# Kernel tuning notes

Hardware: AMD Instinct MI355X
Metric: run time of the kernel (lower is better)

## Reference

```python
import jax, jax.numpy as jnp
import numpy as np
from jax import lax

SEQ, B, NF, NC, D, NO, L = 2036, 32, 64, 100, 512, 4, 2048
EPS = 1e-5


def leaky(x):
    return jnp.where(x > 0, x, 0.2 * x)


def conv1d(x, w, b):
    # x: [B, Cin, L], w: [Cout, Cin, K] -> [B, Cout, L-K+1] (VALID)
    y = lax.conv_general_dilated(x, w, (1,), 'VALID',
                                 dimension_numbers=('NCH', 'OIH', 'NCH'))
    return y + b[None, :, None]


def maxpool3(x):
    # kernel 3, stride 1, VALID, over last dim
    return lax.reduce_window(x, -jnp.inf, lax.max, (1, 1, 3), (1, 1, 1), 'VALID')


def layernorm(x, g, b):
    m = jnp.mean(x, -1, keepdims=True)
    v = jnp.mean(jnp.square(x - m), -1, keepdims=True)
    return (x - m) * lax.rsqrt(v + EPS) * g + b


def setup_inputs() -> dict:
    key = jax.random.key(0)
    ks = jax.random.split(key, 16)
    s = 0.02
    return {
        'input': jax.random.normal(ks[0], (SEQ, B, NF), jnp.float32),
        'history': jax.random.normal(ks[1], (B, NO, L), jnp.float32),
        'static': jax.random.normal(ks[2], (B, NC), jnp.float32),
        'W_feat': jax.random.normal(ks[3], (D, NF), jnp.float32) * s,
        'b_feat': jnp.zeros((D,), jnp.float32),
        'w1': jax.random.normal(ks[4], (D // 4, NO, 3), jnp.float32) * s,
        'b1': jnp.zeros((D // 4,), jnp.float32),
        'w2': jax.random.normal(ks[5], (D // 2, D // 4, 3), jnp.float32) * s,
        'b2': jnp.zeros((D // 2,), jnp.float32),
        'w3': jax.random.normal(ks[6], (D, D // 2, 3), jnp.float32) * s,
        'b3': jnp.zeros((D,), jnp.float32),
        'g1': jnp.ones((D,), jnp.float32),
        'beta1': jnp.zeros((D,), jnp.float32),
        'W_city': jax.random.normal(ks[7], (D, NC), jnp.float32) * s,
        'b_city': jnp.zeros((D,), jnp.float32),
        'g2': jnp.ones((D,), jnp.float32),
        'beta2': jnp.zeros((D,), jnp.float32),
    }


def reference(input, history, static, W_feat, b_feat, w1, b1, w2, b2, w3, b3,
              g1, beta1, W_city, b_city, g2, beta2):
    # feat embed: [S, B, NF] @ [NF, D]
    x = leaky(jnp.einsum('sbf,df->sbd', input, W_feat) + b_feat)
    # conv/pool stack on history [B, NO, L]
    h = maxpool3(leaky(conv1d(history, w1, b1)))
    h = maxpool3(leaky(conv1d(h, w2, b2)))
    h = maxpool3(leaky(conv1d(h, w3, b3)))            # [B, D, S]
    x = x + jnp.transpose(h, (2, 0, 1))               # [S, B, D]
    x = layernorm(x, g1, beta1)
    # diag_embed(city_embed(static)) matmul == broadcasted elementwise scale
    c = static @ W_city.T + b_city                    # [B, D]
    x = x * c[None, :, :]
    x = layernorm(x, g2, beta2)
    return x
```

## Files before the change

kernel.cpp:

```cpp
#include <hip/hip_runtime.h>
#include <hip/hip_bf16.h>

#define SEQ 2036
#define BB 32
#define DDIM 512
#define PREP_BLOCKS 2112

typedef __attribute__((ext_vector_type(4))) float f32x4;
typedef __attribute__((ext_vector_type(8))) short bf16x8v;
typedef __attribute__((ext_vector_type(8))) unsigned short u16x8;
typedef __attribute__((ext_vector_type(4))) unsigned short u16x4;

__device__ __forceinline__ float leaky_f(float x) { return x > 0.f ? x : 0.2f * x; }
__device__ __forceinline__ unsigned short f2bf(float x) {
    unsigned u = __float_as_uint(x);
    return (unsigned short)((u + 0x7fffu + ((u >> 16) & 1u)) >> 16);
}
__device__ __forceinline__ float bf2f(unsigned short h) { return __uint_as_float(((unsigned)h) << 16); }

#define GLOAD_LDS16(g, l)                                                                  \
    __builtin_amdgcn_global_load_lds((__attribute__((address_space(1))) const unsigned int*)(g), \
                                     (__attribute__((address_space(3))) unsigned int*)(l), 16, 0, 0)

__global__ __launch_bounds__(256) void pre_kernel(
    const float* __restrict__ w2, __hip_bfloat16* __restrict__ w2P,
    const float* __restrict__ w3, __hip_bfloat16* __restrict__ wb3,
    const float* __restrict__ Wf, __hip_bfloat16* __restrict__ wfP,
    const float* __restrict__ st, const float* __restrict__ Wc,
    const float* __restrict__ bc, float* __restrict__ cv,
    const float* __restrict__ hist, const float* __restrict__ w1,
    const float* __restrict__ b1, __hip_bfloat16* __restrict__ h1)
{
    __shared__ float t1[4][68];
    const int t = threadIdx.x;
    if (blockIdx.x < PREP_BLOCKS) {
        int idx = blockIdx.x * 256 + t;
        if (idx < 98304) {
            int o = idx & 4095, tile = idx >> 12;
            int nb = tile % 2;
            int tmp = tile / 2;
            int q = tmp % 4, k = tmp / 4;
            int n = o >> 5, low = o & 31;
            int cs = low >> 3, j = low & 7;
            int c = cs ^ ((n >> 1) & 3);
            int kk = (c << 3) | j;
            float v = w2[((size_t)(nb * 128 + n)) * 128 * 3 + (q * 32 + kk) * 3 + k];
            ((unsigned short*)w2P)[idx] = f2bf(v);
            return;
        }
        idx -= 98304;
        if (idx < 393216) {
            int e = idx & 7;
            int l = (idx >> 3) & 63;
            int nf = (idx >> 9) & 3;
            int wn = (idx >> 11) & 1;
            int rest = idx >> 12;
            int nb = rest % 4, ss = rest / 4;
            int k = (ss % 12) >> 2;
            int qg = (ss / 12) * 4 + (ss & 3);
            int n = nb * 128 + wn * 64 + nf * 16 + (l & 15);
            int cin = qg * 32 + (l >> 4) * 8 + e;
            ((unsigned short*)wb3)[idx] = f2bf(w3[(size_t)n * 256 * 3 + cin * 3 + k]);
            return;
        }
        idx -= 393216;
        if (idx < 32768) {
            int e = idx & 7;
            int l = (idx >> 3) & 63;
            int frag = idx >> 9;
            int q = frag >> 5, j = frag & 31;
            int n = l & 15, g = l >> 4;
            ((unsigned short*)wfP)[idx] = f2bf(Wf[(j * 16 + n) * 64 + q * 32 + g * 8 + e]);
            return;
        }
        idx -= 32768;
        if (idx < 16384) {
            int b = idx >> 9, d = idx & 511;
            const float* sb = st + b * 100;
            float acc = bc[d];
#pragma unroll 4
            for (int f = 0; f < 100; ++f) acc = fmaf(sb[f], Wc[d * 100 + f], acc);
            cv[b * 512 + d] = acc;
        }
        return;
    }
    const int cb = blockIdx.x - PREP_BLOCKS;
    const int b = cb >> 5, tile = cb & 31;
    const int d = t & 127, sub = t >> 7;
    const int sbase = tile * 64;
    const float* inb = hist + (size_t)b * 4 * 2048;
    for (int i = t; i < 4 * 68; i += 256) {
        int cin = i / 68, p = i - cin * 68;
        int s = sbase + p;
        t1[cin][p] = (s < 2048) ? inb[cin * 2048 + s] : 0.f;
    }
    __syncthreads();
    float acc[34];
#pragma unroll
    for (int i = 0; i < 34; ++i) acc[i] = 0.f;
#pragma unroll
    for (int cin = 0; cin < 4; ++cin) {
        float w0 = w1[d * 12 + cin * 3 + 0];
        float w1v = w1[d * 12 + cin * 3 + 1];
        float w2v = w1[d * 12 + cin * 3 + 2];
        float r0 = t1[cin][sub * 32], r1 = t1[cin][sub * 32 + 1];
#pragma unroll
        for (int p = 0; p < 34; ++p) {
            float r2 = t1[cin][sub * 32 + p + 2];
            acc[p] = fmaf(r0, w0, fmaf(r1, w1v, fmaf(r2, w2v, acc[p])));
            r0 = r1; r1 = r2;
        }
    }
    const float bvv = b1[d];
    unsigned short* o16 = (unsigned short*)h1;
#pragma unroll
    for (int i = 0; i < 32; ++i) {
        int sp = sbase + sub * 32 + i;
        if (sp < 2044) {
            float v = leaky_f(fmaxf(fmaxf(acc[i], acc[i + 1]), acc[i + 2]) + bvv);
            o16[((size_t)b * 2044 + sp) * 128 + d] = f2bf(v);
        }
    }
}

template <int CIN, int DOUT, bool LDSB>
__global__ __launch_bounds__(256, LDSB ? 3 : 4) void conv_mfma_kernel(
    const __hip_bfloat16* __restrict__ hin,
    const __hip_bfloat16* __restrict__ wprep,
    const float* __restrict__ bias,
    __hip_bfloat16* __restrict__ hout,
    int Lin, int Lpool, long bstride, long sstride)
{
    constexpr int NQ = CIN / 32;
    constexpr int HALVES = (CIN + 127) / 128;
    constexpr int NSTEP = 3 * NQ;
    constexpr int SPH = NSTEP / HALVES;
    constexpr int NBL = DOUT / 128;
    constexpr int SMEM = LDSB ? (34816 + 16384) : 34816;

    __shared__ __attribute__((aligned(16))) unsigned char smem[SMEM];
    unsigned char* panel = smem;
    unsigned char* cstage = smem;
    unsigned char* bls = smem + 34816;

    const int t = threadIdx.x;
    const int lane = t & 63, w = t >> 6;
    const int wr = w >> 1, wn = w & 1;
    const int l15 = lane & 15, lg = lane >> 4;

    const int nwg = gridDim.x;
    const int lw = (blockIdx.x & 7) * (nwg >> 3) + (blockIdx.x >> 3);
    const int nb = lw % NBL;
    const int tmp = lw / NBL;
    const int st = tmp % 17;
    const int b = tmp / 17;
    const int s0 = st * 126;

    auto stage_panel = [&](int half) {
        const char* srcb = (const char*)hin + (((size_t)b * Lin) * CIN + half * 128) * 2;
#pragma unroll
        for (int iter = 0; iter < 8; ++iter) {
            int chunk = iter * 256 + t;
            int r = chunk >> 4, cd = chunk & 15;
            int c = (cd & 8) | ((cd ^ r) & 7);
            int row = s0 + r; if (row > Lin - 1) row = Lin - 1;
            const char* src = srcb + ((size_t)row * CIN + c * 8) * 2;
            GLOAD_LDS16(src, panel + (iter * 256 + w * 64) * 16);
        }
        if (t < 32) {
            int chunk = 2048 + t;
            int r = chunk >> 4, cd = chunk & 15;
            int c = (cd & 8) | ((cd ^ r) & 7);
            int row = s0 + r; if (row > Lin - 1) row = Lin - 1;
            const char* src = srcb + ((size_t)row * CIN + c * 8) * 2;
            GLOAD_LDS16(src, panel + 2048 * 16);
        }
    };

    f32x4 acc[4][4];
#pragma unroll
    for (int i = 0; i < 4; ++i)
#pragma unroll
        for (int j = 0; j < 4; ++j) acc[i][j] = (f32x4){0.f, 0.f, 0.f, 0.f};

    const int rbse = wr * 64 + l15;

    if (LDSB) {
        auto stage_b = [&](int ss, int bi) {
            int k = (ss % SPH) >> 2;
            int qg = (ss / SPH) * 4 + (ss & 3);
            int tile = (k * NQ + qg) * NBL + nb;
            const char* src = (const char*)wprep + (size_t)tile * 8192;
            char* dst = (char*)bls + bi * 8192;
            GLOAD_LDS16(src + t * 16, dst + (w << 10));
            GLOAD_LDS16(src + 4096 + t * 16, dst + 4096 + (w << 10));
        };
        stage_panel(0);
        stage_b(0, 0);
        __syncthreads();
        int boff[4];
#pragma unroll
        for (int nf = 0; nf < 4; ++nf) {
            int n = wn * 64 + nf * 16 + l15;
            boff[nf] = n * 64 + ((lg ^ ((n >> 1) & 3)) << 4);
        }
        for (int ss = 0; ss < NSTEP; ++ss) {
            const int bi = ss & 1;
            if (ss + 1 < NSTEP) stage_b(ss + 1, bi ^ 1);
            const int k = (ss % SPH) >> 2;
            const int cc = (ss & 3) * 4 + lg;
            bf16x8v a[4], bfr[4];
#pragma unroll
            for (int mf = 0; mf < 4; ++mf) {
                int r = rbse + mf * 16 + k;
                int csw = (cc & 8) | ((cc ^ r) & 7);
                a[mf] = *(const bf16x8v*)(panel + r * 256 + (csw << 4));
            }
#pragma unroll
            for (int nf = 0; nf < 4; ++nf)
                bfr[nf] = *(const bf16x8v*)(bls + bi * 8192 + boff[nf]);
#pragma unroll
            for (int mf = 0; mf < 4; ++mf)
#pragma unroll
                for (int nf = 0; nf < 4; ++nf)
                    acc[mf][nf] = __builtin_amdgcn_mfma_f32_16x16x32_bf16(a[mf], bfr[nf], acc[mf][nf], 0, 0, 0);
            __syncthreads();
            if (HALVES == 2 && ss == SPH - 1) {
                stage_panel(1);
                __syncthreads();
            }
        }
        __syncthreads();
    } else {
        const unsigned short* wbp = (const unsigned short*)wprep;
        auto kstep = [&](int ss) {
            const int k = (ss % SPH) >> 2;
            const int cc = (ss & 3) * 4 + lg;
            const unsigned short* wq =
                wbp + (((size_t)ss * NBL + nb) * 2 + wn) * 2048 + (size_t)lane * 8;
            bf16x8v a[4], bfr[4];
#pragma unroll
            for (int nf = 0; nf < 4; ++nf)
                bfr[nf] = *(const bf16x8v*)(wq + nf * 512);
#pragma unroll
            for (int mf = 0; mf < 4; ++mf) {
                int r = rbse + mf * 16 + k;
                int csw = (cc & 8) | ((cc ^ r) & 7);
                a[mf] = *(const bf16x8v*)(panel + r * 256 + (csw << 4));
            }
#pragma unroll
            for (int mf = 0; mf < 4; ++mf)
#pragma unroll
                for (int nf = 0; nf < 4; ++nf)
                    acc[mf][nf] = __builtin_amdgcn_mfma_f32_16x16x32_bf16(a[mf], bfr[nf], acc[mf][nf], 0, 0, 0);
        };
        stage_panel(0);
        __syncthreads();
        for (int ss = 0; ss < SPH; ++ss) kstep(ss);
        if (HALVES == 2) {
            __syncthreads();
            stage_panel(1);
            __syncthreads();
            for (int ss = SPH; ss < NSTEP; ++ss) kstep(ss);
        }
        __syncthreads();
    }

#pragma unroll
    for (int mf = 0; mf < 4; ++mf) {
        int srow = wr * 64 + mf * 16 + (lg << 2);
#pragma unroll
        for (int nf = 0; nf < 4; ++nf) {
            int n = wn * 64 + nf * 16 + l15;
            f32x4 v = acc[mf][nf];
            unsigned lo = (unsigned)f2bf(v.x) | ((unsigned)f2bf(v.y) << 16);
            unsigned hi = (unsigned)f2bf(v.z) | ((unsigned)f2bf(v.w) << 16);
            *(uint2*)(cstage + (size_t)n * 272 + srow * 2) = make_uint2(lo, hi);
        }
    }
    __syncthreads();

    const int n = t & 127, h = t >> 7;
    const float bv = bias[nb * 128 + n];
    const int SP = (Lpool - s0 < 126) ? (Lpool - s0) : 126;
    const int splo = h ? 63 : 0;
    const int sphim = h ? 126 : 63;
    const int sphi = (SP < sphim) ? SP : sphim;
    const int cbg = h ? 7 : 0, ceg = h ? 16 : 9;
    unsigned short* outp = (unsigned short*)hout;
    const size_t obase = (size_t)b * bstride + (size_t)s0 * sstride + nb * 128 + n;
    float p2 = 0.f, p1 = 0.f;
    for (int j = cbg; j < ceg; ++j) {
        u16x8 ch = *(const u16x8*)(cstage + (size_t)n * 272 + (j << 4));
#pragma unroll
        for (int i = 0; i < 8; ++i) {
            float cur = bf2f(ch[i]);
            int sp = j * 8 + i - 2;
            if (sp >= splo && sp < sphi) {
                float v = fmaxf(fmaxf(p2, p1), cur) + bv;
                outp[obase + (size_t)sp * sstride] = f2bf(leaky_f(v));
            }
            p2 = p1; p1 = cur;
        }
    }
}

#define XSTR 514
__global__ __launch_bounds__(256, 4) void epi_mfma3_kernel(
    const float* __restrict__ input,
    const __hip_bfloat16* __restrict__ wfP,
    const float* __restrict__ bfeat,
    const __hip_bfloat16* __restrict__ h3,
    const float* __restrict__ cvec,
    const float* __restrict__ g1, const float* __restrict__ be1,
    const float* __restrict__ g2, const float* __restrict__ be2,
    float* __restrict__ outp)
{
    __shared__ float x_lds[16 * XSTR];
    const int t = threadIdx.x;
    const int lane = t & 63, w = t >> 6;
    const int l15 = lane & 15, lg = lane >> 4;
    const long r0 = (long)blockIdx.x * 16;

    f32x4 acc[8];
#pragma unroll
    for (int jl = 0; jl < 8; ++jl) acc[jl] = (f32x4){0.f, 0.f, 0.f, 0.f};

    const unsigned short* wp = (const unsigned short*)wfP;
#pragma unroll
    for (int q = 0; q < 2; ++q) {
        const f32x4* ap = (const f32x4*)(input + (r0 + l15) * 64 + q * 32 + lg * 8);
        f32x4 a0 = ap[0];
        f32x4 a1 = ap[1];
        bf16x8v af;
        af[0] = (short)f2bf(a0.x); af[1] = (short)f2bf(a0.y);
        af[2] = (short)f2bf(a0.z); af[3] = (short)f2bf(a0.w);
        af[4] = (short)f2bf(a1.x); af[5] = (short)f2bf(a1.y);
        af[6] = (short)f2bf(a1.z); af[7] = (short)f2bf(a1.w);
#pragma unroll
        for (int jl = 0; jl < 8; ++jl) {
            int frag = q * 32 + w * 8 + jl;
            bf16x8v bfr = *(const bf16x8v*)(wp + ((size_t)frag * 64 + lane) * 8);
            acc[jl] = __builtin_amdgcn_mfma_f32_16x16x32_bf16(af, bfr, acc[jl], 0, 0, 0);
        }
    }

#pragma unroll
    for (int jl = 0; jl < 8; ++jl) {
        int d = (w * 8 + jl) * 16 + l15;
        float bfv = bfeat[d];
#pragma unroll
        for (int i = 0; i < 4; ++i) {
            int row = lg * 4 + i;
            x_lds[row * XSTR + d] = leaky_f(acc[jl][i] + bfv);
        }
    }
    __syncthreads();

    const unsigned short* h3u = (const unsigned short*)h3;
    const int l4 = lane * 4;
    f32x4 g1a = *(const f32x4*)(g1 + l4);
    f32x4 g1b = *(const f32x4*)(g1 + 256 + l4);
    f32x4 b1a = *(const f32x4*)(be1 + l4);
    f32x4 b1b = *(const f32x4*)(be1 + 256 + l4);
    f32x4 g2a = *(const f32x4*)(g2 + l4);
    f32x4 g2b = *(const f32x4*)(g2 + 256 + l4);
    f32x4 b2a = *(const f32x4*)(be2 + l4);
    f32x4 b2b = *(const f32x4*)(be2 + 256 + l4);

    for (int rr = 0; rr < 4; ++rr) {
        int row = w * 4 + rr;
        long r = r0 + row;
        int b = (int)(r & 31);
        f32x4 xa = *(const f32x4*)(x_lds + row * XSTR + l4);
        f32x4 xb = *(const f32x4*)(x_lds + row * XSTR + 256 + l4);
        u16x4 ha = *(const u16x4*)(h3u + r * 512 + l4);
        u16x4 hb = *(const u16x4*)(h3u + r * 512 + 256 + l4);
        float v[8];
        float s = 0.f;
#pragma unroll
        for (int e = 0; e < 4; ++e) {
            v[e] = xa[e] + bf2f(ha[e]);
            v[4 + e] = xb[e] + bf2f(hb[e]);
            s += v[e] + v[4 + e];
        }
#pragma unroll
        for (int off = 32; off; off >>= 1) s += __shfl_xor(s, off);
        float m = s * (1.f / 512.f);
        float vs = 0.f;
#pragma unroll
        for (int j = 0; j < 8; ++j) { float dd = v[j] - m; vs += dd * dd; }
#pragma unroll
        for (int off = 32; off; off >>= 1) vs += __shfl_xor(vs, off);
        float rstd = rsqrtf(vs * (1.f / 512.f) + 1e-5f);

        f32x4 ca = *(const f32x4*)(cvec + b * 512 + l4);
        f32x4 cb = *(const f32x4*)(cvec + b * 512 + 256 + l4);
        float z[8]; float s2 = 0.f;
#pragma unroll
        for (int e = 0; e < 4; ++e) {
            z[e] = ((v[e] - m) * rstd * g1a[e] + b1a[e]) * ca[e];
            z[4 + e] = ((v[4 + e] - m) * rstd * g1b[e] + b1b[e]) * cb[e];
            s2 += z[e] + z[4 + e];
        }
#pragma unroll
        for (int off = 32; off; off >>= 1) s2 += __shfl_xor(s2, off);
        float m2 = s2 * (1.f / 512.f);
        float vs2 = 0.f;
#pragma unroll
        for (int j = 0; j < 8; ++j) { float dd = z[j] - m2; vs2 += dd * dd; }
#pragma unroll
        for (int off = 32; off; off >>= 1) vs2 += __shfl_xor(vs2, off);
        float rstd2 = rsqrtf(vs2 * (1.f / 512.f) + 1e-5f);

        f32x4 oa, ob;
#pragma unroll
        for (int e = 0; e < 4; ++e) {
            oa[e] = (z[e] - m2) * rstd2 * g2a[e] + b2a[e];
            ob[e] = (z[4 + e] - m2) * rstd2 * g2b[e] + b2b[e];
        }
        __builtin_nontemporal_store(oa, (f32x4*)(outp + r * 512 + l4));
        __builtin_nontemporal_store(ob, (f32x4*)(outp + r * 512 + 256 + l4));
    }
}

extern "C" void kernel_launch(void* const* d_in, const int* in_sizes, int n_in,
                              void* d_out, int out_size, void* d_ws, size_t ws_size,
                              hipStream_t stream) {
    const float* input   = (const float*)d_in[0];
    const float* history = (const float*)d_in[1];
    const float* stat    = (const float*)d_in[2];
    const float* W_feat  = (const float*)d_in[3];
    const float* b_feat  = (const float*)d_in[4];
    const float* w1      = (const float*)d_in[5];
    const float* b1      = (const float*)d_in[6];
    const float* w2      = (const float*)d_in[7];
    const float* b2      = (const float*)d_in[8];
    const float* w3      = (const float*)d_in[9];
    const float* b3      = (const float*)d_in[10];
    const float* g1      = (const float*)d_in[11];
    const float* beta1   = (const float*)d_in[12];
    const float* W_city  = (const float*)d_in[13];
    const float* b_city  = (const float*)d_in[14];
    const float* g2      = (const float*)d_in[15];
    const float* beta2   = (const float*)d_in[16];
    float* out = (float*)d_out;

    char* wsb = (char*)d_ws;
    size_t off = 0;
    auto alloc = [&](size_t bytes) {
        void* p = wsb + off;
        off = (off + bytes + 255) & ~(size_t)255;
        return p;
    };
    __hip_bfloat16* h1  = (__hip_bfloat16*)alloc((size_t)BB * 2044 * 128 * 2);
    __hip_bfloat16* h2  = (__hip_bfloat16*)alloc((size_t)BB * 2040 * 256 * 2);
    __hip_bfloat16* h3  = (__hip_bfloat16*)alloc((size_t)SEQ * BB * 512 * 2);
    float*          cv  = (float*)alloc((size_t)BB * DDIM * 4);
    __hip_bfloat16* w2P = (__hip_bfloat16*)alloc((size_t)98304 * 2);
    __hip_bfloat16* wb3 = (__hip_bfloat16*)alloc((size_t)393216 * 2);
    __hip_bfloat16* wfP = (__hip_bfloat16*)alloc((size_t)32768 * 2);

    pre_kernel<<<PREP_BLOCKS + 1024, 256, 0, stream>>>(
        w2, w2P, w3, wb3, W_feat, wfP, stat, W_city, b_city, cv,
        history, w1, b1, h1);

    conv_mfma_kernel<128, 256, true><<<17 * 2 * BB, 256, 0, stream>>>(
        h1, w2P, b2, h2, 2044, 2040, 2040L * 256, 256);
    conv_mfma_kernel<256, 512, false><<<17 * 4 * BB, 256, 0, stream>>>(
        h2, wb3, b3, h3, 2040, 2036, 512, 32L * 512);

    epi_mfma3_kernel<<<(SEQ * BB) / 16, 256, 0, stream>>>(
        input, wfP, b_feat, h3, cv, g1, beta1, g2, beta2, out);
}
```

Measured before the change: 171.0 us.

## Shrink conv tiles to 64 rows with 128-thread blocks reading weights from global

Both conv layers now use one kernel with 128-thread blocks that each cover 62 pooled positions instead of 126. The panel and staging buffers shrink to 18 KB. Conv2 drops its LDS double-buffered weight staging and, like conv3, loads pre-swizzled bf16 fragments straight from global memory. The goal is more blocks, higher occupancy and less LDS and barrier overhead, at the cost of more halo recomputation and more repeated weight reads per output.

```diff
diff --git a/kernel.cpp b/kernel.cpp
--- a/kernel.cpp
+++ b/kernel.cpp
@@ -23,7 +23,7 @@
                                      (__attribute__((address_space(3))) unsigned int*)(l), 16, 0, 0)
 
 __global__ __launch_bounds__(256) void pre_kernel(
-    const float* __restrict__ w2, __hip_bfloat16* __restrict__ w2P,
+    const float* __restrict__ w2, __hip_bfloat16* __restrict__ wb2,
     const float* __restrict__ w3, __hip_bfloat16* __restrict__ wb3,
     const float* __restrict__ Wf, __hip_bfloat16* __restrict__ wfP,
     const float* __restrict__ st, const float* __restrict__ Wc,
@@ -36,16 +36,17 @@
     if (blockIdx.x < PREP_BLOCKS) {
         int idx = blockIdx.x * 256 + t;
         if (idx < 98304) {
-            int o = idx & 4095, tile = idx >> 12;
-            int nb = tile % 2;
-            int tmp = tile / 2;
-            int q = tmp % 4, k = tmp / 4;
-            int n = o >> 5, low = o & 31;
-            int cs = low >> 3, j = low & 7;
-            int c = cs ^ ((n >> 1) & 3);
-            int kk = (c << 3) | j;
-            float v = w2[((size_t)(nb * 128 + n)) * 128 * 3 + (q * 32 + kk) * 3 + k];
-            ((unsigned short*)w2P)[idx] = f2bf(v);
+            int e = idx & 7;
+            int l = (idx >> 3) & 63;
+            int nf = (idx >> 9) & 3;
+            int w = (idx >> 11) & 1;
+            int rest = idx >> 12;
+            int nb = rest % 2, ss = rest / 2;
+            int k = ss >> 2;
+            int qg = ss & 3;
+            int n = nb * 128 + w * 64 + nf * 16 + (l & 15);
+            int cin = qg * 32 + (l >> 4) * 8 + e;
+            ((unsigned short*)wb2)[idx] = f2bf(w2[(size_t)n * 384 + cin * 3 + k]);
             return;
         }
         idx -= 98304;
@@ -53,14 +54,14 @@
             int e = idx & 7;
             int l = (idx >> 3) & 63;
             int nf = (idx >> 9) & 3;
-            int wn = (idx >> 11) & 1;
+            int w = (idx >> 11) & 1;
             int rest = idx >> 12;
             int nb = rest % 4, ss = rest / 4;
             int k = (ss % 12) >> 2;
             int qg = (ss / 12) * 4 + (ss & 3);
-            int n = nb * 128 + wn * 64 + nf * 16 + (l & 15);
+            int n = nb * 128 + w * 64 + nf * 16 + (l & 15);
             int cin = qg * 32 + (l >> 4) * 8 + e;
-            ((unsigned short*)wb3)[idx] = f2bf(w3[(size_t)n * 256 * 3 + cin * 3 + k]);
+            ((unsigned short*)wb3)[idx] = f2bf(w3[(size_t)n * 768 + cin * 3 + k]);
             return;
         }
         idx -= 393216;
@@ -123,57 +124,51 @@
     }
 }
 
-template <int CIN, int DOUT, bool LDSB>
-__global__ __launch_bounds__(256, LDSB ? 3 : 4) void conv_mfma_kernel(
+template <int CIN, int NBL>
+__global__ __launch_bounds__(128, 4) void conv_sm_kernel(
     const __hip_bfloat16* __restrict__ hin,
-    const __hip_bfloat16* __restrict__ wprep,
+    const __hip_bfloat16* __restrict__ wb,
     const float* __restrict__ bias,
     __hip_bfloat16* __restrict__ hout,
     int Lin, int Lpool, long bstride, long sstride)
 {
-    constexpr int NQ = CIN / 32;
-    constexpr int HALVES = (CIN + 127) / 128;
-    constexpr int NSTEP = 3 * NQ;
-    constexpr int SPH = NSTEP / HALVES;
-    constexpr int NBL = DOUT / 128;
-    constexpr int SMEM = LDSB ? (34816 + 16384) : 34816;
-
-    __shared__ __attribute__((aligned(16))) unsigned char smem[SMEM];
+    constexpr int HALVES = CIN / 128;
+    constexpr int NSTEP = 3 * (CIN / 32);
+
+    __shared__ __attribute__((aligned(16))) unsigned char smem[18432];
     unsigned char* panel = smem;
     unsigned char* cstage = smem;
-    unsigned char* bls = smem + 34816;
 
     const int t = threadIdx.x;
     const int lane = t & 63, w = t >> 6;
-    const int wr = w >> 1, wn = w & 1;
     const int l15 = lane & 15, lg = lane >> 4;
 
     const int nwg = gridDim.x;
     const int lw = (blockIdx.x & 7) * (nwg >> 3) + (blockIdx.x >> 3);
     const int nb = lw % NBL;
     const int tmp = lw / NBL;
-    const int st = tmp % 17;
-    const int b = tmp / 17;
-    const int s0 = st * 126;
+    const int st = tmp % 33;
+    const int b = tmp / 33;
+    const int s0 = st * 62;
 
     auto stage_panel = [&](int half) {
         const char* srcb = (const char*)hin + (((size_t)b * Lin) * CIN + half * 128) * 2;
 #pragma unroll
         for (int iter = 0; iter < 8; ++iter) {
-            int chunk = iter * 256 + t;
+            int chunk = iter * 128 + t;
             int r = chunk >> 4, cd = chunk & 15;
             int c = (cd & 8) | ((cd ^ r) & 7);
             int row = s0 + r; if (row > Lin - 1) row = Lin - 1;
             const char* src = srcb + ((size_t)row * CIN + c * 8) * 2;
-            GLOAD_LDS16(src, panel + (iter * 256 + w * 64) * 16);
+            GLOAD_LDS16(src, panel + (iter * 128 + w * 64) * 16);
         }
         if (t < 32) {
-            int chunk = 2048 + t;
+            int chunk = 1024 + t;
             int r = chunk >> 4, cd = chunk & 15;
             int c = (cd & 8) | ((cd ^ r) & 7);
             int row = s0 + r; if (row > Lin - 1) row = Lin - 1;
             const char* src = srcb + ((size_t)row * CIN + c * 8) * 2;
-            GLOAD_LDS16(src, panel + 2048 * 16);
+            GLOAD_LDS16(src, panel + 1024 * 16);
         }
     };
 
@@ -183,120 +178,68 @@
 #pragma unroll
         for (int j = 0; j < 4; ++j) acc[i][j] = (f32x4){0.f, 0.f, 0.f, 0.f};
 
-    const int rbse = wr * 64 + l15;
-
-    if (LDSB) {
-        auto stage_b = [&](int ss, int bi) {
-            int k = (ss % SPH) >> 2;
-            int qg = (ss / SPH) * 4 + (ss & 3);
-            int tile = (k * NQ + qg) * NBL + nb;
-            const char* src = (const char*)wprep + (size_t)tile * 8192;
-            char* dst = (char*)bls + bi * 8192;
-            GLOAD_LDS16(src + t * 16, dst + (w << 10));
-            GLOAD_LDS16(src + 4096 + t * 16, dst + 4096 + (w << 10));
-        };
-        stage_panel(0);
-        stage_b(0, 0);
+    const unsigned short* wbp = (const unsigned short*)wb;
+    auto kstep = [&](int ss) {
+        const int k = (ss % 12) >> 2;
+        const int cc = (ss & 3) * 4 + lg;
+        const unsigned short* wq =
+            wbp + (((size_t)ss * NBL + nb) * 2 + w) * 2048 + (size_t)lane * 8;
+        bf16x8v a[4], bfr[4];
+#pragma unroll
+        for (int nf = 0; nf < 4; ++nf)
+            bfr[nf] = *(const bf16x8v*)(wq + nf * 512);
+#pragma unroll
+        for (int mf = 0; mf < 4; ++mf) {
+            int r = l15 + mf * 16 + k;
+            int csw = (cc & 8) | ((cc ^ r) & 7);
+            a[mf] = *(const bf16x8v*)(panel + r * 256 + (csw << 4));
+        }
+#pragma unroll
+        for (int mf = 0; mf < 4; ++mf)
+#pragma unroll
+            for (int nf = 0; nf < 4; ++nf)
+                acc[mf][nf] = __builtin_amdgcn_mfma_f32_16x16x32_bf16(a[mf], bfr[nf], acc[mf][nf], 0, 0, 0);
+    };
+
+    stage_panel(0);
+    __syncthreads();
+    for (int ss = 0; ss < 12; ++ss) kstep(ss);
+    if (HALVES == 2) {
         __syncthreads();
-        int boff[4];
+        stage_panel(1);
+        __syncthreads();
+        for (int ss = 12; ss < NSTEP; ++ss) kstep(ss);
+    }
+    __syncthreads();
+
+#pragma unroll
+    for (int mf = 0; mf < 4; ++mf) {
+        int srow = mf * 16 + (lg << 2);
 #pragma unroll
         for (int nf = 0; nf < 4; ++nf) {
-            int n = wn * 64 + nf * 16 + l15;
-            boff[nf] = n * 64 + ((lg ^ ((n >> 1) & 3)) << 4);
-        }
-        for (int ss = 0; ss < NSTEP; ++ss) {
-            const int bi = ss & 1;
-            if (ss + 1 < NSTEP) stage_b(ss + 1, bi ^ 1);
-            const int k = (ss % SPH) >> 2;
-            const int cc = (ss & 3) * 4 + lg;
-            bf16x8v a[4], bfr[4];
-#pragma unroll
-            for (int mf = 0; mf < 4; ++mf) {
-                int r = rbse + mf * 16 + k;
-                int csw = (cc & 8) | ((cc ^ r) & 7);
-                a[mf] = *(const bf16x8v*)(panel + r * 256 + (csw << 4));
-            }
-#pragma unroll
-            for (int nf = 0; nf < 4; ++nf)
-                bfr[nf] = *(const bf16x8v*)(bls + bi * 8192 + boff[nf]);
-#pragma unroll
-            for (int mf = 0; mf < 4; ++mf)
-#pragma unroll
-                for (int nf = 0; nf < 4; ++nf)
-                    acc[mf][nf] = __builtin_amdgcn_mfma_f32_16x16x32_bf16(a[mf], bfr[nf], acc[mf][nf], 0, 0, 0);
-            __syncthreads();
-            if (HALVES == 2 && ss == SPH - 1) {
-                stage_panel(1);
-                __syncthreads();
-            }
-        }
-        __syncthreads();
-    } else {
-        const unsigned short* wbp = (const unsigned short*)wprep;
-        auto kstep = [&](int ss) {
-            const int k = (ss % SPH) >> 2;
-            const int cc = (ss & 3) * 4 + lg;
-            const unsigned short* wq =
-                wbp + (((size_t)ss * NBL + nb) * 2 + wn) * 2048 + (size_t)lane * 8;
-            bf16x8v a[4], bfr[4];
-#pragma unroll
-            for (int nf = 0; nf < 4; ++nf)
-                bfr[nf] = *(const bf16x8v*)(wq + nf * 512);
-#pragma unroll
-            for (int mf = 0; mf < 4; ++mf) {
-                int r = rbse + mf * 16 + k;
-                int csw = (cc & 8) | ((cc ^ r) & 7);
-                a[mf] = *(const bf16x8v*)(panel + r * 256 + (csw << 4));
-            }
-#pragma unroll
-            for (int mf = 0; mf < 4; ++mf)
-#pragma unroll
-                for (int nf = 0; nf < 4; ++nf)
-                    acc[mf][nf] = __builtin_amdgcn_mfma_f32_16x16x32_bf16(a[mf], bfr[nf], acc[mf][nf], 0, 0, 0);
-        };
-        stage_panel(0);
-        __syncthreads();
-        for (int ss = 0; ss < SPH; ++ss) kstep(ss);
-        if (HALVES == 2) {
-            __syncthreads();
-            stage_panel(1);
-            __syncthreads();
-            for (int ss = SPH; ss < NSTEP; ++ss) kstep(ss);
-        }
-        __syncthreads();
-    }
-
-#pragma unroll
-    for (int mf = 0; mf < 4; ++mf) {
-        int srow = wr * 64 + mf * 16 + (lg << 2);
-#pragma unroll
-        for (int nf = 0; nf < 4; ++nf) {
-            int n = wn * 64 + nf * 16 + l15;
+            int n = w * 64 + nf * 16 + l15;
             f32x4 v = acc[mf][nf];
             unsigned lo = (unsigned)f2bf(v.x) | ((unsigned)f2bf(v.y) << 16);
             unsigned hi = (unsigned)f2bf(v.z) | ((unsigned)f2bf(v.w) << 16);
-            *(uint2*)(cstage + (size_t)n * 272 + srow * 2) = make_uint2(lo, hi);
+            *(uint2*)(cstage + (size_t)n * 144 + srow * 2) = make_uint2(lo, hi);
         }
     }
     __syncthreads();
 
-    const int n = t & 127, h = t >> 7;
+    const int n = t;
     const float bv = bias[nb * 128 + n];
-    const int SP = (Lpool - s0 < 126) ? (Lpool - s0) : 126;
-    const int splo = h ? 63 : 0;
-    const int sphim = h ? 126 : 63;
-    const int sphi = (SP < sphim) ? SP : sphim;
-    const int cbg = h ? 7 : 0, ceg = h ? 16 : 9;
+    const int SP = (Lpool - s0 < 62) ? (Lpool - s0) : 62;
     unsigned short* outp = (unsigned short*)hout;
     const size_t obase = (size_t)b * bstride + (size_t)s0 * sstride + nb * 128 + n;
     float p2 = 0.f, p1 = 0.f;
-    for (int j = cbg; j < ceg; ++j) {
-        u16x8 ch = *(const u16x8*)(cstage + (size_t)n * 272 + (j << 4));
+#pragma unroll
+    for (int j = 0; j < 8; ++j) {
+        u16x8 ch = *(const u16x8*)(cstage + (size_t)n * 144 + (j << 4));
 #pragma unroll
         for (int i = 0; i < 8; ++i) {
             float cur = bf2f(ch[i]);
             int sp = j * 8 + i - 2;
-            if (sp >= splo && sp < sphi) {
+            if ((unsigned)sp < (unsigned)SP) {
                 float v = fmaxf(fmaxf(p2, p1), cur) + bv;
                 outp[obase + (size_t)sp * sstride] = f2bf(leaky_f(v));
             }
@@ -457,18 +400,19 @@
     __hip_bfloat16* h2  = (__hip_bfloat16*)alloc((size_t)BB * 2040 * 256 * 2);
     __hip_bfloat16* h3  = (__hip_bfloat16*)alloc((size_t)SEQ * BB * 512 * 2);
     float*          cv  = (float*)alloc((size_t)BB * DDIM * 4);
-    __hip_bfloat16* w2P = (__hip_bfloat16*)alloc((size_t)98304 * 2);
+    __hip_bfloat16* wb2 = (__hip_bfloat16*)alloc((size_t)98304 * 2);
     __hip_bfloat16* wb3 = (__hip_bfloat16*)alloc((size_t)393216 * 2);
     __hip_bfloat16* wfP = (__hip_bfloat16*)alloc((size_t)32768 * 2);
 
     pre_kernel<<<PREP_BLOCKS + 1024, 256, 0, stream>>>(
-        w2, w2P, w3, wb3, W_feat, wfP, stat, W_city, b_city, cv,
+        w2, wb2, w3, wb3, W_feat, wfP, stat, W_city, b_city, cv,
         history, w1, b1, h1);
 
-    conv_mfma_kernel<128, 256, true><<<17 * 2 * BB, 256, 0, stream>>>(
-        h1, w2P, b2, h2, 2044, 2040, 2040L * 256, 256);
-    conv_mfma_kernel<256, 512, false><<<17 * 4 * BB, 256, 0, stream>>>(
-        h2, wb3, b3, h3, 2040, 2036, 512, 32L * 512);
+    conv_sm_kernel<128, 2><<<33 * 2 * BB, 128, 0, stream>>>(
+        h1, wb2, b2, h2, 2044, 2040, 2040L * 256, 256);
+
+    conv_sm_kernel<256, 4><<<33 * 4 * BB, 128, 0, stream>>>(
+        h2, wb3, b3, h3, 2040, 2036, 512, 16384);
 
     epi_mfma3_kernel<<<(SEQ * BB) / 16, 256, 0, stream>>>(
         input, wfP, b_feat, h3, cv, g1, beta1, g2, beta2, out);
```

Measured after the change: 178.6 us. +4.5%, slower.
